# Optimization experiments

Hardware: AMD Instinct MI355X
Metric: run time of the kernel (lower is better)

## Reference

```python
import jax, jax.numpy as jnp
import numpy as np

D = 512
H = 8
B, S = 4, 2048


def _layernorm(x, g, b, eps=1e-6):
    m = jnp.mean(x, axis=-1, keepdims=True)
    v = jnp.mean(jnp.square(x - m), axis=-1, keepdims=True)
    return (x - m) * jax.lax.rsqrt(v + eps) * g + b


def setup_inputs() -> dict:
    key = jax.random.key(0)
    ks = jax.random.split(key, 8)
    w = 1.0 / np.sqrt(D)  # glorot-ish scale so softmax doesn't saturate
    return {
        "x": jax.random.normal(ks[0], (B, S, D), dtype=jnp.float32),
        "Q": jax.random.normal(ks[1], (H, D, D), dtype=jnp.float32) * w,
        "K": jax.random.normal(ks[2], (H, D, D), dtype=jnp.float32) * w,
        "g1": jnp.ones((D,), jnp.float32),
        "beta1": jnp.zeros((D,), jnp.float32),
        "Wp": jax.random.normal(ks[3], (H * D, D), dtype=jnp.float32) / np.sqrt(H * D),
        "bp": jnp.zeros((D,), jnp.float32),
        "g2": jnp.ones((D,), jnp.float32),
        "beta2": jnp.zeros((D,), jnp.float32),
        "W1": jax.random.normal(ks[4], (D, 4 * D), dtype=jnp.float32) * w,
        "b1": jnp.zeros((4 * D,), jnp.float32),
        "W2": jax.random.normal(ks[5], (4 * D, D), dtype=jnp.float32) / np.sqrt(4 * D),
        "b2": jnp.zeros((D,), jnp.float32),
    }


def reference(x, Q, K, g1, beta1, Wp, bp, g2, beta2, W1, b1, W2, b2):
    # layernorm1
    xn = _layernorm(x, g1, beta1)  # [B,S,D]
    # per-head attention, batched over heads via einsum
    Qx = jnp.einsum("bsd,hde->hbse", xn, Q)  # [H,B,S,D]
    Kx = jnp.einsum("bsd,hde->hbse", xn, K)  # [H,B,S,D]
    scale = 1.0 / jnp.sqrt(jnp.float32(D))
    A = jnp.einsum("hbse,hbte->hbst", Qx, Kx) * scale  # [H,B,S,S]
    A = jax.nn.softmax(A, axis=-1)
    head = jnp.einsum("hbst,btd->hbsd", A, xn) + xn  # per-head residual
    # concat heads along last axis: order h0,h1,... -> [B,S,H*D]
    cat = jnp.transpose(head, (1, 2, 0, 3)).reshape(x.shape[0], x.shape[1], -1)
    # projection
    y = cat @ Wp + bp  # [B,S,D]
    # layernorm2
    y = _layernorm(y, g2, beta2)
    # MLP with residual, exact gelu (keras default)
    h = jax.nn.gelu(y @ W1 + b1, approximate=False)
    h = jax.nn.gelu(h @ W2 + b2, approximate=False)
    return y + h
```

## Files before the change

### kernel.cpp

```cpp
#include <hip/hip_runtime.h>

using u16 = unsigned short;
typedef u16 u16x8 __attribute__((ext_vector_type(8)));
typedef __bf16 bf16x8 __attribute__((ext_vector_type(8)));
typedef float f32x4 __attribute__((ext_vector_type(4)));

__device__ __forceinline__ u16 f2bf(float f) {
  unsigned u = __builtin_bit_cast(unsigned, f);
  u += 0x7fffu + ((u >> 16) & 1u);
  return (u16)(u >> 16);
}
__device__ __forceinline__ float bf2f(u16 h) {
  unsigned u = ((unsigned)h) << 16;
  return __builtin_bit_cast(float, u);
}
__device__ __forceinline__ f32x4 mfma16(u16x8 a, u16x8 b, f32x4 c) {
  return __builtin_amdgcn_mfma_f32_16x16x32_bf16(
      __builtin_bit_cast(bf16x8, a), __builtin_bit_cast(bf16x8, b), c, 0, 0, 0);
}
__device__ __forceinline__ float gelu_f(float v) {
  return 0.5f * v * (1.0f + erff(v * 0.70710678118654752f));
}
__device__ __forceinline__ void gll16(const u16* g, u16* l) {
  __builtin_amdgcn_global_load_lds(
      (const __attribute__((address_space(1))) unsigned*)g,
      (__attribute__((address_space(3))) unsigned*)l, 16, 0, 0);
}

__device__ __forceinline__ float loadf(const float* p) { return *p; }
__device__ __forceinline__ float loadf(const u16* p) { return bf2f(*p); }

template <typename T>
__global__ void tcast_kernel(const T* __restrict__ in, u16* __restrict__ out, int R, int C,
                             float scale) {
  __shared__ float tile[32][33];
  const T* ip = in + (size_t)blockIdx.z * R * C;
  u16* op = out + (size_t)blockIdx.z * R * C;
  int c0 = blockIdx.x * 32, r0 = blockIdx.y * 32;
  int tx = threadIdx.x, ty = threadIdx.y;
#pragma unroll
  for (int i = 0; i < 32; i += 8)
    tile[ty + i][tx] = loadf(ip + (size_t)(r0 + ty + i) * C + (c0 + tx));
  __syncthreads();
#pragma unroll
  for (int i = 0; i < 32; i += 8)
    op[(size_t)(c0 + ty + i) * R + (r0 + tx)] = f2bf(tile[tx][ty + i] * scale);
}

__global__ void vtile_kernel(const u16* __restrict__ in, u16* __restrict__ out) {
  __shared__ u16 tile[32][33];
  const int b = blockIdx.z;
  const int d0 = blockIdx.x * 32, t0 = blockIdx.y * 32;
  const int tx = threadIdx.x, ty = threadIdx.y;
  const u16* ip = in + (size_t)b * 2048 * 512;
#pragma unroll
  for (int i = 0; i < 32; i += 8)
    tile[ty + i][tx] = ip[(size_t)(t0 + ty + i) * 512 + d0 + tx];
  __syncthreads();
  u16* op = out + ((size_t)b * 64 + (t0 >> 5)) * 16384;
#pragma unroll
  for (int i = 0; i < 32; i += 8) {
    const int d = d0 + ty + i;
    op[(size_t)(tx >> 3) * 4096 + (size_t)d * 8 + (tx & 7)] = tile[tx][ty + i];
  }
}

__global__ __launch_bounds__(256) void ln_kernel(
    const float* __restrict__ x, const float* __restrict__ g, const float* __restrict__ b,
    u16* __restrict__ obf, float* __restrict__ of32) {
  const int D = 512;
  int row = blockIdx.x;
  const float* xr = x + (size_t)row * D;
  float2 v = ((const float2*)xr)[threadIdx.x];
  float s = v.x + v.y;
#pragma unroll
  for (int o = 1; o < 64; o <<= 1) s += __shfl_xor(s, o);
  __shared__ float red[4];
  int wid = threadIdx.x >> 6;
  if ((threadIdx.x & 63) == 0) red[wid] = s;
  __syncthreads();
  float mean = (red[0] + red[1] + red[2] + red[3]) * (1.0f / D);
  float dx = v.x - mean, dy = v.y - mean;
  float q = dx * dx + dy * dy;
#pragma unroll
  for (int o = 1; o < 64; o <<= 1) q += __shfl_xor(q, o);
  __syncthreads();
  if ((threadIdx.x & 63) == 0) red[wid] = q;
  __syncthreads();
  float var = (red[0] + red[1] + red[2] + red[3]) * (1.0f / D);
  float rstd = rsqrtf(var + 1e-6f);
  int c = threadIdx.x * 2;
  float o0 = dx * rstd * g[c] + b[c];
  float o1 = dy * rstd * g[c + 1] + b[c + 1];
  obf[(size_t)row * D + c] = f2bf(o0);
  obf[(size_t)row * D + c + 1] = f2bf(o1);
  if (of32 != nullptr) {
    of32[(size_t)row * D + c] = o0;
    of32[(size_t)row * D + c + 1] = o1;
  }
}

__global__ __launch_bounds__(256) void gemm_kernel(
    const u16* __restrict__ A, const u16* __restrict__ Bt,
    const float* __restrict__ bias, const float* __restrict__ resid,
    void* __restrict__ Cout, int M, int N, int K, int mode,
    size_t sA, size_t sB, size_t sC, size_t aHS) {
  __shared__ u16 As[128 * 64];
  __shared__ u16 Bs[128 * 64];
  A += (size_t)blockIdx.z * sA;
  Bt += (size_t)blockIdx.z * sB;
  const size_t zC = (size_t)blockIdx.z * sC;
  const int m0 = blockIdx.y * 128, n0 = blockIdx.x * 128;
  const int tid = threadIdx.x;
  const int l = tid & 63, wv = tid >> 6;
  const int wr = (wv >> 1) * 64, wc = (wv & 1) * 64;
  const int lr = l & 15, lq = l >> 4;
  const int srow = l >> 3;
  const int sc = l & 7;
  f32x4 z4 = {0.f, 0.f, 0.f, 0.f};
  f32x4 acc[4][4];
#pragma unroll
  for (int mi = 0; mi < 4; mi++)
#pragma unroll
    for (int ni = 0; ni < 4; ni++) acc[mi][ni] = z4;

  for (int k0 = 0; k0 < K; k0 += 64) {
    __syncthreads();
#pragma unroll
    for (int j = 0; j < 4; ++j) {
      const int r = wv * 32 + j * 8 + srow;
      const int kc = (sc ^ (r & 7)) * 8;
      const u16* asrc;
      if (aHS) asrc = A + (size_t)(k0 >> 9) * aHS + (size_t)(m0 + r) * 512 + ((k0 & 511) + kc);
      else asrc = A + (size_t)(m0 + r) * K + k0 + kc;
      gll16(asrc, &As[(wv * 32 + j * 8) * 64]);
      const u16* bsrc = Bt + (size_t)(n0 + r) * K + k0 + kc;
      gll16(bsrc, &Bs[(wv * 32 + j * 8) * 64]);
    }
    asm volatile("s_waitcnt vmcnt(0)" ::: "memory");
    __syncthreads();
#pragma unroll
    for (int kk = 0; kk < 2; ++kk) {
      const int rc = ((kk * 4 + lq) ^ (lr & 7)) * 8;
      u16x8 af[4], bfr[4];
#pragma unroll
      for (int mi = 0; mi < 4; mi++) af[mi] = *(const u16x8*)&As[(wr + mi * 16 + lr) * 64 + rc];
#pragma unroll
      for (int ni = 0; ni < 4; ni++) bfr[ni] = *(const u16x8*)&Bs[(wc + ni * 16 + lr) * 64 + rc];
#pragma unroll
      for (int mi = 0; mi < 4; mi++)
#pragma unroll
        for (int ni = 0; ni < 4; ni++) acc[mi][ni] = mfma16(af[mi], bfr[ni], acc[mi][ni]);
    }
  }
#pragma unroll
  for (int mi = 0; mi < 4; mi++) {
#pragma unroll
    for (int ni = 0; ni < 4; ni++) {
      const int gn = n0 + wc + ni * 16 + lr;
      const float bv = (mode != 0 && bias != nullptr) ? bias[gn] : 0.0f;
#pragma unroll
      for (int r = 0; r < 4; r++) {
        const int gm = m0 + wr + mi * 16 + (l >> 4) * 4 + r;
        float v = acc[mi][ni][r];
        const size_t idx = zC + (size_t)gm * N + gn;
        if (mode == 0) ((u16*)Cout)[idx] = f2bf(v);
        else if (mode == 1) ((float*)Cout)[idx] = v + bv;
        else if (mode == 2) ((u16*)Cout)[idx] = f2bf(gelu_f(v + bv));
        else ((float*)Cout)[idx] = gelu_f(v + bv) + resid[(size_t)gm * N + gn];
      }
    }
  }
}

__global__ __launch_bounds__(512, 2) void flash_kernel(
    const u16* __restrict__ Qx, const u16* __restrict__ Kx,
    const u16* __restrict__ xnTt, const u16* __restrict__ xn,
    u16* __restrict__ headout) {
  __shared__ u16 Ks[2][32][512];
  __shared__ u16 Ps[128][40];
  __shared__ float fLds[128];
  __shared__ float lLds[128];

  const int tid = threadIdx.x;
  const int l = tid & 63, wv = tid >> 6;
  const int lr = l & 15, lq = l >> 4, lk8 = lq * 8;
  const int r7 = lr & 7;
  const int h = blockIdx.y >> 2, b = blockIdx.y & 3;
  const int s0 = blockIdx.x * 128;
  const size_t rowHB = (size_t)h * 8192 + (size_t)b * 2048;
  const u16* Qbase = Qx + (rowHB + s0) * 512;
  const u16* Kbase = Kx + rowHB * 512;
  const u16* Vbatch = xnTt + (size_t)b * 64 * 16384;
  const u16* xnb = xn + ((size_t)b * 2048 + s0) * 512;

  u16x8 q[16];
  {
    const u16* qr = Qbase + (size_t)(wv * 16 + lr) * 512 + lk8;
#pragma unroll
    for (int ks = 0; ks < 16; ks++) q[ks] = *(const u16x8*)(qr + ks * 32);
  }
  f32x4 z4 = {0.f, 0.f, 0.f, 0.f};
  f32x4 o[8][4];
#pragma unroll
  for (int mi = 0; mi < 8; mi++)
#pragma unroll
    for (int ni = 0; ni < 4; ni++) o[mi][ni] = z4;
  float m_r[4], l_r[4];
#pragma unroll
  for (int r = 0; r < 4; r++) { m_r[r] = -1e30f; l_r[r] = 0.f; }

#define STAGE(buf, tt0)                                                      \
  do {                                                                       \
    _Pragma("unroll") for (int j = 0; j < 4; ++j) {                          \
      const int row_ = wv * 4 + j;                                           \
      gll16(Kbase + (size_t)((tt0) + row_) * 512 + ((l ^ (row_ & 7)) * 8),   \
            &Ks[buf][row_][0]);                                              \
    }                                                                        \
  } while (0)

  STAGE(0, 0);
  for (int it = 0; it < 64; ++it) {
    const int cur = it & 1;
    asm volatile("s_waitcnt vmcnt(0)" ::: "memory");
    __builtin_amdgcn_s_barrier();
    __builtin_amdgcn_sched_barrier(0);
    STAGE(cur ^ 1, (size_t)((it + 1) & 63) * 32);
    __builtin_amdgcn_sched_barrier(0);
    f32x4 sv0 = z4, sv1 = z4;
    __builtin_amdgcn_s_setprio(1);
#pragma unroll
    for (int ks = 0; ks < 16; ks++) {
      const int col = (((ks << 2) | lq) ^ r7) << 3;
      u16x8 kb0 = *(const u16x8*)&Ks[cur][lr][col];
      u16x8 kb1 = *(const u16x8*)&Ks[cur][16 + lr][col];
      sv0 = mfma16(q[ks], kb0, sv0);
      sv1 = mfma16(q[ks], kb1, sv1);
    }
    __builtin_amdgcn_s_setprio(0);
    float tm[4], fac[4];
#pragma unroll
    for (int r = 0; r < 4; r++) tm[r] = fmaxf(sv0[r], sv1[r]);
#pragma unroll
    for (int r = 0; r < 4; r++) {
      tm[r] = fmaxf(tm[r], __shfl_xor(tm[r], 1));
      tm[r] = fmaxf(tm[r], __shfl_xor(tm[r], 2));
      tm[r] = fmaxf(tm[r], __shfl_xor(tm[r], 4));
      tm[r] = fmaxf(tm[r], __shfl_xor(tm[r], 8));
    }
#pragma unroll
    for (int r = 0; r < 4; r++) {
      float mn = fmaxf(m_r[r], tm[r]);
      fac[r] = __expf(m_r[r] - mn);
      m_r[r] = mn;
      float p0 = __expf(sv0[r] - mn);
      float p1 = __expf(sv1[r] - mn);
      const int prow = wv * 16 + lq * 4 + r;
      Ps[prow][lr] = f2bf(p0);
      Ps[prow][16 + lr] = f2bf(p1);
      float rs = p0 + p1;
      rs += __shfl_xor(rs, 1);
      rs += __shfl_xor(rs, 2);
      rs += __shfl_xor(rs, 4);
      rs += __shfl_xor(rs, 8);
      l_r[r] = l_r[r] * fac[r] + rs;
    }
    if (lr == 0) {
#pragma unroll
      for (int r = 0; r < 4; r++) fLds[wv * 16 + lq * 4 + r] = fac[r];
    }
    asm volatile("s_waitcnt lgkmcnt(0)" ::: "memory");
    __builtin_amdgcn_s_barrier();
    __builtin_amdgcn_sched_barrier(0);
    const u16* Vt_ = Vbatch + (size_t)it * 16384;
    u16x8 vb[4];
#pragma unroll
    for (int ni = 0; ni < 4; ni++)
      vb[ni] = *(const u16x8*)(Vt_ + lq * 4096 + (size_t)(wv * 64 + ni * 16 + lr) * 8);
    __builtin_amdgcn_sched_barrier(0);
#pragma unroll
    for (int mi = 0; mi < 8; mi++) {
#pragma unroll
      for (int r = 0; r < 4; r++) {
        const float fv = fLds[mi * 16 + lq * 4 + r];
#pragma unroll
        for (int ni = 0; ni < 4; ni++) o[mi][ni][r] *= fv;
      }
    }
    asm volatile("s_waitcnt vmcnt(4)" ::: "memory");
    __builtin_amdgcn_sched_barrier(0);
    __builtin_amdgcn_s_setprio(1);
#pragma unroll
    for (int mi = 0; mi < 8; mi++) {
      u16x8 pa = *(const u16x8*)&Ps[mi * 16 + lr][lk8];
#pragma unroll
      for (int ni = 0; ni < 4; ni++) o[mi][ni] = mfma16(pa, vb[ni], o[mi][ni]);
    }
    __builtin_amdgcn_s_setprio(0);
  }
#undef STAGE
  asm volatile("s_waitcnt vmcnt(0)" ::: "memory");
  if (lr == 0) {
#pragma unroll
    for (int r = 0; r < 4; r++) lLds[wv * 16 + lq * 4 + r] = l_r[r];
  }
  __syncthreads();
  u16* outp = headout + (rowHB + s0) * 512;
#pragma unroll
  for (int mi = 0; mi < 8; mi++) {
#pragma unroll
    for (int r = 0; r < 4; r++) {
      const int row = mi * 16 + lq * 4 + r;
      const float linv = 1.0f / lLds[row];
      const u16* xr = xnb + (size_t)row * 512;
      u16* orow = outp + (size_t)row * 512;
#pragma unroll
      for (int ni = 0; ni < 4; ni++) {
        const int c = wv * 64 + ni * 16 + lr;
        orow[c] = f2bf(o[mi][ni][r] * linv + bf2f(xr[c]));
      }
    }
  }
}

extern "C" void kernel_launch(void* const* d_in, const int* in_sizes, int n_in,
                              void* d_out, int out_size, void* d_ws, size_t ws_size,
                              hipStream_t stream) {
  (void)in_sizes; (void)n_in; (void)out_size; (void)ws_size;
  const float* x   = (const float*)d_in[0];
  const float* Qw  = (const float*)d_in[1];
  const float* Kw  = (const float*)d_in[2];
  const float* g1  = (const float*)d_in[3];
  const float* be1 = (const float*)d_in[4];
  const float* Wp  = (const float*)d_in[5];
  const float* bp  = (const float*)d_in[6];
  const float* g2  = (const float*)d_in[7];
  const float* be2 = (const float*)d_in[8];
  const float* W1  = (const float*)d_in[9];
  const float* b1  = (const float*)d_in[10];
  const float* W2  = (const float*)d_in[11];
  const float* b2  = (const float*)d_in[12];
  float* out = (float*)d_out;

  u16* ws = (u16*)d_ws;
  size_t off = 0;
  u16* Qt   = ws + off; off += 8ull * 512 * 512;
  u16* Kt   = ws + off; off += 8ull * 512 * 512;
  u16* Wpt  = ws + off; off += 512ull * 4096;
  u16* W1t  = ws + off; off += 2048ull * 512;
  u16* W2t  = ws + off; off += 512ull * 2048;
  u16* xnb  = ws + off; off += 8192ull * 512;
  u16* xnTt = ws + off; off += 4ull * 512 * 2048;
  u16* Qx   = ws + off; off += 8ull * 8192 * 512;
  u16* Kx   = ws + off; off += 8ull * 8192 * 512;
  u16* yn   = ws + off; off += 8192ull * 512;
  float* y   = (float*)(ws + off); off += 8192ull * 512 * 2;
  float* ynf = (float*)(ws + off); off += 8192ull * 512 * 2;
  u16* h1 = Qx;

  const float qscale = 0.04419417382415922f;
  dim3 tb(32, 8);
  tcast_kernel<float><<<dim3(16, 16, 8), tb, 0, stream>>>(Qw, Qt, 512, 512, qscale);
  tcast_kernel<float><<<dim3(16, 16, 8), tb, 0, stream>>>(Kw, Kt, 512, 512, 1.0f);
  tcast_kernel<float><<<dim3(16, 128, 1), tb, 0, stream>>>(Wp, Wpt, 4096, 512, 1.0f);
  tcast_kernel<float><<<dim3(64, 16, 1), tb, 0, stream>>>(W1, W1t, 512, 2048, 1.0f);
  tcast_kernel<float><<<dim3(16, 64, 1), tb, 0, stream>>>(W2, W2t, 2048, 512, 1.0f);
  ln_kernel<<<8192, 256, 0, stream>>>(x, g1, be1, xnb, nullptr);
  vtile_kernel<<<dim3(16, 64, 4), tb, 0, stream>>>(xnb, xnTt);
  gemm_kernel<<<dim3(4, 64, 8), 256, 0, stream>>>(xnb, Qt, nullptr, nullptr, Qx,
      8192, 512, 512, 0, 0, 262144, 4194304, 0);
  gemm_kernel<<<dim3(4, 64, 8), 256, 0, stream>>>(xnb, Kt, nullptr, nullptr, Kx,
      8192, 512, 512, 0, 0, 262144, 4194304, 0);
  flash_kernel<<<dim3(16, 32), 512, 0, stream>>>(Qx, Kx, xnTt, xnb, Qx);
  gemm_kernel<<<dim3(4, 64, 1), 256, 0, stream>>>(Qx, Wpt, bp, nullptr, y,
      8192, 512, 4096, 1, 0, 0, 0, 4194304);
  ln_kernel<<<8192, 256, 0, stream>>>(y, g2, be2, yn, ynf);
  gemm_kernel<<<dim3(16, 64, 1), 256, 0, stream>>>(yn, W1t, b1, nullptr, h1,
      8192, 2048, 512, 2, 0, 0, 0, 0);
  gemm_kernel<<<dim3(4, 64, 1), 256, 0, stream>>>(h1, W2t, b2, ynf, out,
      8192, 512, 2048, 3, 0, 0, 0, 0);
}
```

Before: 941.0 us.

## Skip softmax rescaling when row max is unchanged and single-buffer K tiles

The flash attention loop now checks, per wave, whether any new score exceeds the running row maximum. If none does, it skips the max shuffle-reductions, the correction exponentials and the rescale of the output accumulator, and a shared flag lets all waves agree on skipping the rescale. Row sums are kept as per-lane partials and reduced once at the end instead of every iteration. The K tile moves from double to single buffering, which halves that LDS use, but the next K load now overlaps only the PV matmul and each iteration ends with an extra wait and barrier.

```diff
diff --git a/kernel.cpp b/kernel.cpp
--- a/kernel.cpp
+++ b/kernel.cpp
@@ -177,10 +177,11 @@
     const u16* __restrict__ Qx, const u16* __restrict__ Kx,
     const u16* __restrict__ xnTt, const u16* __restrict__ xn,
     u16* __restrict__ headout) {
-  __shared__ u16 Ks[2][32][512];
+  __shared__ u16 Ks[32][512];
   __shared__ u16 Ps[128][40];
   __shared__ float fLds[128];
   __shared__ float lLds[128];
+  __shared__ unsigned flagLds[8];
 
   const int tid = threadIdx.x;
   const int l = tid & 63, wv = tid >> 6;
@@ -210,65 +211,71 @@
 #pragma unroll
   for (int r = 0; r < 4; r++) { m_r[r] = -1e30f; l_r[r] = 0.f; }
 
-#define STAGE(buf, tt0)                                                      \
+#define STAGE(tt0)                                                           \
   do {                                                                       \
     _Pragma("unroll") for (int j = 0; j < 4; ++j) {                          \
       const int row_ = wv * 4 + j;                                           \
       gll16(Kbase + (size_t)((tt0) + row_) * 512 + ((l ^ (row_ & 7)) * 8),   \
-            &Ks[buf][row_][0]);                                              \
+            &Ks[row_][0]);                                                   \
     }                                                                        \
   } while (0)
 
-  STAGE(0, 0);
+  STAGE(0);
+  asm volatile("s_waitcnt vmcnt(0)" ::: "memory");
+  __builtin_amdgcn_s_barrier();
   for (int it = 0; it < 64; ++it) {
-    const int cur = it & 1;
-    asm volatile("s_waitcnt vmcnt(0)" ::: "memory");
-    __builtin_amdgcn_s_barrier();
-    __builtin_amdgcn_sched_barrier(0);
-    STAGE(cur ^ 1, (size_t)((it + 1) & 63) * 32);
     __builtin_amdgcn_sched_barrier(0);
     f32x4 sv0 = z4, sv1 = z4;
     __builtin_amdgcn_s_setprio(1);
 #pragma unroll
     for (int ks = 0; ks < 16; ks++) {
       const int col = (((ks << 2) | lq) ^ r7) << 3;
-      u16x8 kb0 = *(const u16x8*)&Ks[cur][lr][col];
-      u16x8 kb1 = *(const u16x8*)&Ks[cur][16 + lr][col];
+      u16x8 kb0 = *(const u16x8*)&Ks[lr][col];
+      u16x8 kb1 = *(const u16x8*)&Ks[16 + lr][col];
       sv0 = mfma16(q[ks], kb0, sv0);
       sv1 = mfma16(q[ks], kb1, sv1);
     }
     __builtin_amdgcn_s_setprio(0);
-    float tm[4], fac[4];
-#pragma unroll
-    for (int r = 0; r < 4; r++) tm[r] = fmaxf(sv0[r], sv1[r]);
-#pragma unroll
-    for (int r = 0; r < 4; r++) {
-      tm[r] = fmaxf(tm[r], __shfl_xor(tm[r], 1));
-      tm[r] = fmaxf(tm[r], __shfl_xor(tm[r], 2));
-      tm[r] = fmaxf(tm[r], __shfl_xor(tm[r], 4));
-      tm[r] = fmaxf(tm[r], __shfl_xor(tm[r], 8));
-    }
-#pragma unroll
-    for (int r = 0; r < 4; r++) {
-      float mn = fmaxf(m_r[r], tm[r]);
-      fac[r] = __expf(m_r[r] - mn);
-      m_r[r] = mn;
-      float p0 = __expf(sv0[r] - mn);
-      float p1 = __expf(sv1[r] - mn);
-      const int prow = wv * 16 + lq * 4 + r;
-      Ps[prow][lr] = f2bf(p0);
-      Ps[prow][16 + lr] = f2bf(p1);
-      float rs = p0 + p1;
-      rs += __shfl_xor(rs, 1);
-      rs += __shfl_xor(rs, 2);
-      rs += __shfl_xor(rs, 4);
-      rs += __shfl_xor(rs, 8);
-      l_r[r] = l_r[r] * fac[r] + rs;
-    }
-    if (lr == 0) {
-#pragma unroll
-      for (int r = 0; r < 4; r++) fLds[wv * 16 + lq * 4 + r] = fac[r];
-    }
+    bool okl = true;
+#pragma unroll
+    for (int r = 0; r < 4; r++)
+      okl = okl && (sv0[r] <= m_r[r]) && (sv1[r] <= m_r[r]);
+    const bool allok = __all((int)okl);
+    if (allok) {
+#pragma unroll
+      for (int r = 0; r < 4; r++) {
+        float p0 = __expf(sv0[r] - m_r[r]);
+        float p1 = __expf(sv1[r] - m_r[r]);
+        l_r[r] += p0 + p1;
+        const int prow = wv * 16 + lq * 4 + r;
+        Ps[prow][lr] = f2bf(p0);
+        Ps[prow][16 + lr] = f2bf(p1);
+      }
+      if (lr == 0) {
+#pragma unroll
+        for (int r = 0; r < 4; r++) fLds[wv * 16 + lq * 4 + r] = 1.0f;
+      }
+    } else {
+#pragma unroll
+      for (int r = 0; r < 4; r++) {
+        float tm = fmaxf(sv0[r], sv1[r]);
+        tm = fmaxf(tm, __shfl_xor(tm, 1));
+        tm = fmaxf(tm, __shfl_xor(tm, 2));
+        tm = fmaxf(tm, __shfl_xor(tm, 4));
+        tm = fmaxf(tm, __shfl_xor(tm, 8));
+        float mn = fmaxf(m_r[r], tm);
+        float fac = __expf(m_r[r] - mn);
+        m_r[r] = mn;
+        float p0 = __expf(sv0[r] - mn);
+        float p1 = __expf(sv1[r] - mn);
+        l_r[r] = l_r[r] * fac + p0 + p1;
+        const int prow = wv * 16 + lq * 4 + r;
+        Ps[prow][lr] = f2bf(p0);
+        Ps[prow][16 + lr] = f2bf(p1);
+        if (lr == 0) fLds[prow] = fac;
+      }
+    }
+    if (l == 0) flagLds[wv] = allok ? 1u : 0u;
     asm volatile("s_waitcnt lgkmcnt(0)" ::: "memory");
     __builtin_amdgcn_s_barrier();
     __builtin_amdgcn_sched_barrier(0);
@@ -277,14 +284,20 @@
 #pragma unroll
     for (int ni = 0; ni < 4; ni++)
       vb[ni] = *(const u16x8*)(Vt_ + lq * 4096 + (size_t)(wv * 64 + ni * 16 + lr) * 8);
+    STAGE((size_t)((it + 1) & 63) * 32);
     __builtin_amdgcn_sched_barrier(0);
-#pragma unroll
-    for (int mi = 0; mi < 8; mi++) {
-#pragma unroll
-      for (int r = 0; r < 4; r++) {
-        const float fv = fLds[mi * 16 + lq * 4 + r];
-#pragma unroll
-        for (int ni = 0; ni < 4; ni++) o[mi][ni][r] *= fv;
+    unsigned allf = 1;
+#pragma unroll
+    for (int w = 0; w < 8; ++w) allf &= flagLds[w];
+    if (allf == 0) {
+#pragma unroll
+      for (int mi = 0; mi < 8; mi++) {
+#pragma unroll
+        for (int r = 0; r < 4; r++) {
+          const float fv = fLds[mi * 16 + lq * 4 + r];
+#pragma unroll
+          for (int ni = 0; ni < 4; ni++) o[mi][ni][r] *= fv;
+        }
       }
     }
     asm volatile("s_waitcnt vmcnt(4)" ::: "memory");
@@ -297,12 +310,18 @@
       for (int ni = 0; ni < 4; ni++) o[mi][ni] = mfma16(pa, vb[ni], o[mi][ni]);
     }
     __builtin_amdgcn_s_setprio(0);
+    asm volatile("s_waitcnt vmcnt(0)" ::: "memory");
+    __builtin_amdgcn_s_barrier();
   }
 #undef STAGE
-  asm volatile("s_waitcnt vmcnt(0)" ::: "memory");
-  if (lr == 0) {
-#pragma unroll
-    for (int r = 0; r < 4; r++) lLds[wv * 16 + lq * 4 + r] = l_r[r];
+#pragma unroll
+  for (int r = 0; r < 4; r++) {
+    float s = l_r[r];
+    s += __shfl_xor(s, 1);
+    s += __shfl_xor(s, 2);
+    s += __shfl_xor(s, 4);
+    s += __shfl_xor(s, 8);
+    if (lr == 0) lLds[wv * 16 + lq * 4 + r] = s;
   }
   __syncthreads();
   u16* outp = headout + (rowHB + s0) * 512;
```

Result: slower. 1.038 ms (+10.3%).

## Double flash KV tile to 64 keys and merge Q/K projection launches

Applied to the files above, without the earlier changes.

The flash attention kernel now processes 64 keys per iteration instead of 32. That halves the loop trip count and the barriers per key, and the next K tile is staged after the V-fragment loads so the copy overlaps the PV MFMAs. Separately, the Q and K projection GEMMs become one launch over 16 z-slices, relying on Qt/Kt and Qx/Kx sitting contiguously in the workspace. The larger K double-buffer and P tile raise LDS use to roughly 147KB per block, which likely drops flash occupancy from two blocks per CU to one.

```diff
diff --git a/kernel.cpp b/kernel.cpp
--- a/kernel.cpp
+++ b/kernel.cpp
@@ -177,8 +177,8 @@
     const u16* __restrict__ Qx, const u16* __restrict__ Kx,
     const u16* __restrict__ xnTt, const u16* __restrict__ xn,
     u16* __restrict__ headout) {
-  __shared__ u16 Ks[2][32][512];
-  __shared__ u16 Ps[128][40];
+  __shared__ u16 Ks[2][64][512];
+  __shared__ u16 Ps[128][72];
   __shared__ float fLds[128];
   __shared__ float lLds[128];
 
@@ -212,37 +212,37 @@
 
 #define STAGE(buf, tt0)                                                      \
   do {                                                                       \
-    _Pragma("unroll") for (int j = 0; j < 4; ++j) {                          \
-      const int row_ = wv * 4 + j;                                           \
+    _Pragma("unroll") for (int j = 0; j < 8; ++j) {                          \
+      const int row_ = wv * 8 + j;                                           \
       gll16(Kbase + (size_t)((tt0) + row_) * 512 + ((l ^ (row_ & 7)) * 8),   \
             &Ks[buf][row_][0]);                                              \
     }                                                                        \
   } while (0)
 
   STAGE(0, 0);
-  for (int it = 0; it < 64; ++it) {
+  for (int it = 0; it < 32; ++it) {
     const int cur = it & 1;
     asm volatile("s_waitcnt vmcnt(0)" ::: "memory");
     __builtin_amdgcn_s_barrier();
     __builtin_amdgcn_sched_barrier(0);
-    STAGE(cur ^ 1, (size_t)((it + 1) & 63) * 32);
-    __builtin_amdgcn_sched_barrier(0);
-    f32x4 sv0 = z4, sv1 = z4;
+    f32x4 sv[4];
+#pragma unroll
+    for (int tq = 0; tq < 4; tq++) sv[tq] = z4;
     __builtin_amdgcn_s_setprio(1);
 #pragma unroll
     for (int ks = 0; ks < 16; ks++) {
       const int col = (((ks << 2) | lq) ^ r7) << 3;
-      u16x8 kb0 = *(const u16x8*)&Ks[cur][lr][col];
-      u16x8 kb1 = *(const u16x8*)&Ks[cur][16 + lr][col];
-      sv0 = mfma16(q[ks], kb0, sv0);
-      sv1 = mfma16(q[ks], kb1, sv1);
+#pragma unroll
+      for (int tq = 0; tq < 4; tq++) {
+        u16x8 kb = *(const u16x8*)&Ks[cur][tq * 16 + lr][col];
+        sv[tq] = mfma16(q[ks], kb, sv[tq]);
+      }
     }
     __builtin_amdgcn_s_setprio(0);
     float tm[4], fac[4];
 #pragma unroll
-    for (int r = 0; r < 4; r++) tm[r] = fmaxf(sv0[r], sv1[r]);
-#pragma unroll
     for (int r = 0; r < 4; r++) {
+      tm[r] = fmaxf(fmaxf(sv[0][r], sv[1][r]), fmaxf(sv[2][r], sv[3][r]));
       tm[r] = fmaxf(tm[r], __shfl_xor(tm[r], 1));
       tm[r] = fmaxf(tm[r], __shfl_xor(tm[r], 2));
       tm[r] = fmaxf(tm[r], __shfl_xor(tm[r], 4));
@@ -253,12 +253,14 @@
       float mn = fmaxf(m_r[r], tm[r]);
       fac[r] = __expf(m_r[r] - mn);
       m_r[r] = mn;
-      float p0 = __expf(sv0[r] - mn);
-      float p1 = __expf(sv1[r] - mn);
       const int prow = wv * 16 + lq * 4 + r;
-      Ps[prow][lr] = f2bf(p0);
-      Ps[prow][16 + lr] = f2bf(p1);
-      float rs = p0 + p1;
+      float rs = 0.f;
+#pragma unroll
+      for (int tq = 0; tq < 4; tq++) {
+        float p = __expf(sv[tq][r] - mn);
+        rs += p;
+        Ps[prow][tq * 16 + lr] = f2bf(p);
+      }
       rs += __shfl_xor(rs, 1);
       rs += __shfl_xor(rs, 2);
       rs += __shfl_xor(rs, 4);
@@ -269,14 +271,18 @@
 #pragma unroll
       for (int r = 0; r < 4; r++) fLds[wv * 16 + lq * 4 + r] = fac[r];
     }
+    const u16* Vt0 = Vbatch + (size_t)(2 * it) * 16384;
+    u16x8 vb0[4], vb1[4];
+#pragma unroll
+    for (int ni = 0; ni < 4; ni++)
+      vb0[ni] = *(const u16x8*)(Vt0 + lq * 4096 + (size_t)(wv * 64 + ni * 16 + lr) * 8);
+#pragma unroll
+    for (int ni = 0; ni < 4; ni++)
+      vb1[ni] = *(const u16x8*)(Vt0 + 16384 + lq * 4096 + (size_t)(wv * 64 + ni * 16 + lr) * 8);
     asm volatile("s_waitcnt lgkmcnt(0)" ::: "memory");
     __builtin_amdgcn_s_barrier();
     __builtin_amdgcn_sched_barrier(0);
-    const u16* Vt_ = Vbatch + (size_t)it * 16384;
-    u16x8 vb[4];
-#pragma unroll
-    for (int ni = 0; ni < 4; ni++)
-      vb[ni] = *(const u16x8*)(Vt_ + lq * 4096 + (size_t)(wv * 64 + ni * 16 + lr) * 8);
+    STAGE(cur ^ 1, (size_t)((it + 1) & 31) * 64);
     __builtin_amdgcn_sched_barrier(0);
 #pragma unroll
     for (int mi = 0; mi < 8; mi++) {
@@ -287,14 +293,20 @@
         for (int ni = 0; ni < 4; ni++) o[mi][ni][r] *= fv;
       }
     }
-    asm volatile("s_waitcnt vmcnt(4)" ::: "memory");
+    asm volatile("s_waitcnt vmcnt(8)" ::: "memory");
     __builtin_amdgcn_sched_barrier(0);
     __builtin_amdgcn_s_setprio(1);
 #pragma unroll
     for (int mi = 0; mi < 8; mi++) {
       u16x8 pa = *(const u16x8*)&Ps[mi * 16 + lr][lk8];
 #pragma unroll
-      for (int ni = 0; ni < 4; ni++) o[mi][ni] = mfma16(pa, vb[ni], o[mi][ni]);
+      for (int ni = 0; ni < 4; ni++) o[mi][ni] = mfma16(pa, vb0[ni], o[mi][ni]);
+    }
+#pragma unroll
+    for (int mi = 0; mi < 8; mi++) {
+      u16x8 pa = *(const u16x8*)&Ps[mi * 16 + lr][32 + lk8];
+#pragma unroll
+      for (int ni = 0; ni < 4; ni++) o[mi][ni] = mfma16(pa, vb1[ni], o[mi][ni]);
     }
     __builtin_amdgcn_s_setprio(0);
   }
@@ -367,9 +379,7 @@
   tcast_kernel<float><<<dim3(16, 64, 1), tb, 0, stream>>>(W2, W2t, 2048, 512, 1.0f);
   ln_kernel<<<8192, 256, 0, stream>>>(x, g1, be1, xnb, nullptr);
   vtile_kernel<<<dim3(16, 64, 4), tb, 0, stream>>>(xnb, xnTt);
-  gemm_kernel<<<dim3(4, 64, 8), 256, 0, stream>>>(xnb, Qt, nullptr, nullptr, Qx,
-      8192, 512, 512, 0, 0, 262144, 4194304, 0);
-  gemm_kernel<<<dim3(4, 64, 8), 256, 0, stream>>>(xnb, Kt, nullptr, nullptr, Kx,
+  gemm_kernel<<<dim3(4, 64, 16), 256, 0, stream>>>(xnb, Qt, nullptr, nullptr, Qx,
       8192, 512, 512, 0, 0, 262144, 4194304, 0);
   flash_kernel<<<dim3(16, 32), 512, 0, stream>>>(Qx, Kx, xnTt, xnb, Qx);
   gemm_kernel<<<dim3(4, 64, 1), 256, 0, stream>>>(Qx, Wpt, bp, nullptr, y,
```

Measured after the change: 1.197 ms. 1.27x slower.
